# Kernel tuning notes

Hardware: AMD Instinct MI355X
Metric: run time of the kernel (lower is better)

## Reference

```python
import jax, jax.numpy as jnp
import numpy as np

TEMPERATURE = 34.0
PAD = 1  # kernel_size // 2

def setup_inputs() -> dict:
    key = jax.random.key(0)
    ks = jax.random.split(key, 5)
    B, C, H, W = 32, 256, 56, 56
    K, O, I, kh = 4, 256, 256, 3
    hidden = int(C * 0.25) + 1  # 65
    return {
        "x": jax.random.normal(ks[0], (B, C, H, W), jnp.float32),
        "fc1_w": jax.random.normal(ks[1], (hidden, C), jnp.float32) * (2.0 / C) ** 0.5,
        "fc2_w": jax.random.normal(ks[2], (K, hidden), jnp.float32) * (2.0 / hidden) ** 0.5,
        "fc2_b": jnp.zeros((K,), jnp.float32),
        "weight": jax.random.normal(ks[3], (K, O, I, kh, kh), jnp.float32) * (2.0 / (I * kh * kh)) ** 0.5,
        "bias": jnp.zeros((K, O), jnp.float32),
    }

def reference(x, fc1_w, fc2_w, fc2_b, weight, bias):
    # attention2d: global avg pool -> 1x1 conv (fc1) -> relu -> 1x1 conv (fc2) -> softmax(logits/T)
    pooled = x.mean(axis=(2, 3))                      # [B, C]
    h = jax.nn.relu(pooled @ fc1_w.T)                 # [B, hidden]
    logits = h @ fc2_w.T + fc2_b                      # [B, K]
    att = jax.nn.softmax(logits / TEMPERATURE, axis=1)
    # aggregate per-sample conv weights/bias over K kernel banks
    agg_w = jnp.einsum('bk,koihw->boihw', att, weight)  # [B, O, I, kh, kw]
    agg_b = att @ bias                                  # [B, O]
    # per-sample conv (torch emulates via groups=B): vmap over batch
    def conv_one(xi, wi):
        return jax.lax.conv_general_dilated(
            xi[None], wi, window_strides=(1, 1),
            padding=((PAD, PAD), (PAD, PAD)),
            dimension_numbers=('NCHW', 'OIHW', 'NCHW'))[0]
    out = jax.vmap(conv_one)(x, agg_w)                 # [B, O, H, W]
    return out + agg_b[:, :, None, None]
```

## Files before the change

### kernel.cpp

```cpp
#include <hip/hip_runtime.h>


typedef short bf16x8 __attribute__((ext_vector_type(8)));
typedef float f32x16 __attribute__((ext_vector_type(16)));

__device__ __forceinline__ unsigned short f2bf(float f) {
  unsigned int u = __float_as_uint(f);
  return (unsigned short)((u + 0x7FFFu + ((u >> 16) & 1u)) >> 16);
}
__device__ __forceinline__ float bf2f(unsigned short h) {
  return __uint_as_float(((unsigned int)h) << 16);
}

__device__ __forceinline__ int invswz(int S) {
  int b7 = (S >> 7) & 1;
  int b6 = ((S >> 6) & 1) ^ b7;
  int b5 = ((S >> 5) & 1) ^ b6;
  int b4 = ((S >> 4) & 1) ^ b5;
  return (S & ~0x70) | (b4 << 4) | (b5 << 5) | (b6 << 6);
}

typedef const __attribute__((address_space(1))) unsigned int* gas_t;
typedef __attribute__((address_space(3))) unsigned int* las_t;
__device__ __forceinline__ void dma16(const void* g, unsigned lds_addr) {
  __builtin_amdgcn_global_load_lds((gas_t)g, (las_t)(size_t)lds_addr, 16, 0, 0);
}

__global__ void xcast_k(const float* __restrict__ x, unsigned short* __restrict__ xb,
                        float* __restrict__ pooled) {
  __shared__ unsigned short tile[64 * 260];
  int b = blockIdx.y;
  int hw0 = blockIdx.x * 64;
  int t = threadIdx.x;
  int p = t & 15, g = t >> 4;
#pragma unroll
  for (int i = 0; i < 16; ++i) {
    int c = g + 16 * i;
    float4 v = *(const float4*)(x + ((size_t)(b * 256 + c)) * 3136 + hw0 + p * 4);
    tile[(p * 4 + 0) * 260 + c] = f2bf(v.x);
    tile[(p * 4 + 1) * 260 + c] = f2bf(v.y);
    tile[(p * 4 + 2) * 260 + c] = f2bf(v.z);
    tile[(p * 4 + 3) * 260 + c] = f2bf(v.w);
  }
  __syncthreads();
  int lane = t & 63, wq = t >> 6;
  int c4 = lane * 4;
#pragma unroll
  for (int it = 0; it < 16; ++it) {
    int hl = it * 4 + wq;
    ushort4 v = *(const ushort4*)&tile[hl * 260 + c4];
    *(ushort4*)&xb[((size_t)(b * 3136 + hw0 + hl)) * 256 + c4] = v;
  }
  float s = 0.f;
#pragma unroll 16
  for (int hl = 0; hl < 64; ++hl) s += bf2f(tile[hl * 260 + t]);
  atomicAdd(&pooled[b * 256 + t], s * (1.0f / 3136.0f));
}

__global__ void att_k(const float* __restrict__ pooled, const float* __restrict__ fc1,
                      const float* __restrict__ fc2w, const float* __restrict__ fc2b,
                      const float* __restrict__ bias, float* __restrict__ att,
                      float* __restrict__ aggb) {
  int b = blockIdx.x, t = threadIdx.x;
  __shared__ float p[256];
  __shared__ float h[65];
  __shared__ float a4[4];
  for (int i = t; i < 256; i += 64) p[i] = pooled[b * 256 + i];
  __syncthreads();
  for (int j = t; j < 65; j += 64) {
    float s = 0.f;
    for (int c = 0; c < 256; ++c) s += p[c] * fc1[j * 256 + c];
    h[j] = fmaxf(s, 0.f);
  }
  __syncthreads();
  if (t == 0) {
    float lg[4];
    for (int k = 0; k < 4; ++k) {
      float s = fc2b[k];
      for (int j = 0; j < 65; ++j) s += h[j] * fc2w[k * 65 + j];
      lg[k] = s * (1.0f / 34.0f);
    }
    float m = fmaxf(fmaxf(lg[0], lg[1]), fmaxf(lg[2], lg[3]));
    float e0 = expf(lg[0] - m), e1 = expf(lg[1] - m), e2 = expf(lg[2] - m), e3 = expf(lg[3] - m);
    float inv = 1.0f / (e0 + e1 + e2 + e3);
    a4[0] = e0 * inv; a4[1] = e1 * inv; a4[2] = e2 * inv; a4[3] = e3 * inv;
    for (int k = 0; k < 4; ++k) att[b * 4 + k] = a4[k];
  }
  __syncthreads();
  for (int o = t; o < 256; o += 64) {
    float s = 0.f;
    for (int k = 0; k < 4; ++k) s += a4[k] * bias[k * 256 + o];
    aggb[b * 256 + o] = s;
  }
}

__global__ void aggw_k(const float* __restrict__ weight, const float* __restrict__ att,
                       unsigned short* __restrict__ aggw) {
  __shared__ float wl[4 * 2304];
  int o = blockIdx.x, t = threadIdx.x;
  for (int k = 0; k < 4; ++k)
    for (int idx = t; idx < 2304; idx += 256)
      wl[k * 2304 + idx] = weight[((size_t)(k * 256 + o)) * 2304 + idx];
  __syncthreads();
  int ot = o >> 7, ol = o & 127, ic = t >> 4, il = t & 15;
  int b0 = blockIdx.y * 8;
  for (int b = b0; b < b0 + 8; ++b) {
    float a0 = att[b * 4 + 0], a1 = att[b * 4 + 1], a2 = att[b * 4 + 2], a3 = att[b * 4 + 3];
    size_t base = ((size_t)((b * 2 + ot) * 16 + ic)) * (9 * 2048) + ol * 16 + il;
#pragma unroll
    for (int r = 0; r < 9; ++r) {
      float s = a0 * wl[t * 9 + r] + a1 * wl[2304 + t * 9 + r] +
                a2 * wl[4608 + t * 9 + r] + a3 * wl[6912 + t * 9 + r];
      aggw[base + r * 2048] = f2bf(s);
    }
  }
}

#define XBUF 16384

__global__ __launch_bounds__(256, 2) void conv_k(const unsigned short* __restrict__ xb,
                                                 const unsigned short* __restrict__ aggw,
                                                 const float* __restrict__ aggb,
                                                 const float* __restrict__ zerobuf,
                                                 float* __restrict__ out) {
  __shared__ __align__(16) unsigned char lds[2 * XBUF];
  const unsigned ldsbase = (unsigned)(size_t)&lds[0];
  const int t = threadIdx.x;
  const int wid = t >> 6, lane = t & 63, l31 = lane & 31, q = lane >> 5;
  const int wo = wid >> 1, wn = wid & 1;

  int id = blockIdx.x;
  int wgid = (id & 7) * 104 + (id >> 3);
  int bn = wgid % 13;
  int rest = wgid / 13;
  int b = rest >> 1, bo = rest & 1;

  const int o0 = bo * 128;
  const int n0 = bn * 256;
  const int h0 = n0 / 56;

  int bbase[4], nn[4], swz[4][3];
#pragma unroll
  for (int nf = 0; nf < 4; ++nf) {
    int n = n0 + wn * 128 + nf * 32 + l31;
    int h = n / 56, w = n - h * 56;
    nn[nf] = n;
    bbase[nf] = ((h - h0) * 64 + w) * 32 + q * 16;
#pragma unroll
    for (int dw = 0; dw < 3; ++dw) swz[nf][dw] = ((w + dw) & 7) << 4;
  }
  int aoff[2];
#pragma unroll
  for (int mf = 0; mf < 2; ++mf) aoff[mf] = (wo * 64 + mf * 32 + l31) * 32 + q * 16;

  const char* xb_b = (const char*)xb + (size_t)b * 3136 * 512;
  const char* ag_c = (const char*)aggw + (size_t)rest * 589824;

  const char* xg[4];
#pragma unroll
  for (int j = 0; j < 4; ++j) {
    int S = (j * 256 + t) * 16;
    int L = invswz(S);
    int pos = L >> 5, sub = (L >> 4) & 1;
    int row = pos >> 6, col = pos & 63;
    int hg = h0 - 1 + row, wg = col - 1;
    bool valid = (col >= 1 && col <= 56 && hg >= 0 && hg < 56);
    xg[j] = valid ? (xb_b + (size_t)(hg * 56 + wg) * 512 + sub * 16) : (const char*)zerobuf;
  }

  f32x16 acc[2][4];
#pragma unroll
  for (int i = 0; i < 2; ++i)
#pragma unroll
    for (int j = 0; j < 4; ++j)
#pragma unroll
      for (int e = 0; e < 16; ++e) acc[i][j][e] = 0.f;

#pragma unroll
  for (int j = 0; j < 4; ++j) dma16(xg[j], ldsbase + j * 4096 + wid * 1024);
  __syncthreads();

  int cur = 0;
  for (int ic = 0; ic < 16; ++ic) {
    bf16x8 areg[2][9];
    const char* agc = ag_c + (size_t)ic * 36864;
#pragma unroll
    for (int r = 0; r < 9; ++r) {
      areg[0][r] = *(const bf16x8*)(agc + r * 4096 + aoff[0]);
      areg[1][r] = *(const bf16x8*)(agc + r * 4096 + aoff[1]);
    }
    if (ic + 1 < 16) {
#pragma unroll
      for (int j = 0; j < 4; ++j)
        dma16(xg[j] + (ic + 1) * 32, ldsbase + (cur ^ 1) * XBUF + j * 4096 + wid * 1024);
    }
    __builtin_amdgcn_sched_barrier(0);
    const unsigned char* xlds = lds + cur * XBUF;
#pragma unroll
    for (int r = 0; r < 9; ++r) {
      const int dh = r / 3, dw = r % 3;
      bf16x8 b0 = *(const bf16x8*)(xlds + ((bbase[0] + dh * 2048 + dw * 32) ^ swz[0][dw]));
      bf16x8 b1 = *(const bf16x8*)(xlds + ((bbase[1] + dh * 2048 + dw * 32) ^ swz[1][dw]));
      bf16x8 b2 = *(const bf16x8*)(xlds + ((bbase[2] + dh * 2048 + dw * 32) ^ swz[2][dw]));
      bf16x8 b3 = *(const bf16x8*)(xlds + ((bbase[3] + dh * 2048 + dw * 32) ^ swz[3][dw]));
      __builtin_amdgcn_s_setprio(1);
      acc[0][0] = __builtin_amdgcn_mfma_f32_32x32x16_bf16(areg[0][r], b0, acc[0][0], 0, 0, 0);
      acc[0][1] = __builtin_amdgcn_mfma_f32_32x32x16_bf16(areg[0][r], b1, acc[0][1], 0, 0, 0);
      acc[0][2] = __builtin_amdgcn_mfma_f32_32x32x16_bf16(areg[0][r], b2, acc[0][2], 0, 0, 0);
      acc[0][3] = __builtin_amdgcn_mfma_f32_32x32x16_bf16(areg[0][r], b3, acc[0][3], 0, 0, 0);
      acc[1][0] = __builtin_amdgcn_mfma_f32_32x32x16_bf16(areg[1][r], b0, acc[1][0], 0, 0, 0);
      acc[1][1] = __builtin_amdgcn_mfma_f32_32x32x16_bf16(areg[1][r], b1, acc[1][1], 0, 0, 0);
      acc[1][2] = __builtin_amdgcn_mfma_f32_32x32x16_bf16(areg[1][r], b2, acc[1][2], 0, 0, 0);
      acc[1][3] = __builtin_amdgcn_mfma_f32_32x32x16_bf16(areg[1][r], b3, acc[1][3], 0, 0, 0);
      __builtin_amdgcn_s_setprio(0);
    }
    __syncthreads();
    cur ^= 1;
  }

#pragma unroll
  for (int mf = 0; mf < 2; ++mf) {
#pragma unroll
    for (int reg = 0; reg < 16; ++reg) {
      int o = o0 + wo * 64 + mf * 32 + (reg & 3) + 8 * (reg >> 2) + 4 * q;
      float ab = aggb[b * 256 + o];
      float* op = out + ((size_t)(b * 256 + o)) * 3136;
#pragma unroll
      for (int nf = 0; nf < 4; ++nf) {
        if (nn[nf] < 3136) op[nn[nf]] = acc[mf][nf][reg] + ab;
      }
    }
  }
}

extern "C" void kernel_launch(void* const* d_in, const int* in_sizes, int n_in,
                              void* d_out, int out_size, void* d_ws, size_t ws_size,
                              hipStream_t stream) {
  const float* x      = (const float*)d_in[0];
  const float* fc1    = (const float*)d_in[1];
  const float* fc2w   = (const float*)d_in[2];
  const float* fc2b   = (const float*)d_in[3];
  const float* weight = (const float*)d_in[4];
  const float* bias   = (const float*)d_in[5];
  float* out = (float*)d_out;

  char* ws = (char*)d_ws;
  float* pooled         = (float*)(ws);
  float* att            = (float*)(ws + 32768);
  float* aggb           = (float*)(ws + 33280);
  unsigned short* aggw  = (unsigned short*)(ws + 66048);
  unsigned short* xb    = (unsigned short*)(ws + 66048 + 37748736);

  hipMemsetAsync(pooled, 0, 32768, stream);
  xcast_k<<<dim3(49, 32), 256, 0, stream>>>(x, xb, pooled);
  att_k<<<32, 64, 0, stream>>>(pooled, fc1, fc2w, fc2b, bias, att, aggb);
  hipMemsetAsync(pooled, 0, 1024, stream);
  aggw_k<<<dim3(256, 4), 256, 0, stream>>>(weight, att, aggw);
  conv_k<<<832, 256, 0, stream>>>(xb, aggw, aggb, (const float*)pooled, out);
}
```

Measured before the change: 257.1 us.

## Triple-buffer input tiles in LDS and stream weight fragments per tap

Moves the LDS staging of input activations from double to triple buffering, prefetching two channel chunks ahead and waiting only with a partial vmcnt instead of a full syncthreads. The weight fragments are no longer loaded all at once (18 registers of bf16x8) but software-pipelined one tap ahead, which cuts register pressure. The aim is to hide global-memory latency behind MFMA work and keep occupancy, at the cost of 48KB of LDS per block, which may limit blocks per CU. The hand-written vmcnt counting is fragile: the weight global loads also count toward vmcnt, so correctness depends on the compiler's ordering.

```diff
diff --git a/kernel.cpp b/kernel.cpp
--- a/kernel.cpp
+++ b/kernel.cpp
@@ -123,7 +123,7 @@
                                                  const float* __restrict__ aggb,
                                                  const float* __restrict__ zerobuf,
                                                  float* __restrict__ out) {
-  __shared__ __align__(16) unsigned char lds[2 * XBUF];
+  __shared__ __align__(16) unsigned char lds[3 * XBUF];
   const unsigned ldsbase = (unsigned)(size_t)&lds[0];
   const int t = threadIdx.x;
   const int wid = t >> 6, lane = t & 63, l31 = lane & 31, q = lane >> 5;
@@ -178,45 +178,56 @@
 
 #pragma unroll
   for (int j = 0; j < 4; ++j) dma16(xg[j], ldsbase + j * 4096 + wid * 1024);
-  __syncthreads();
+#pragma unroll
+  for (int j = 0; j < 4; ++j) dma16(xg[j] + 32, ldsbase + XBUF + j * 4096 + wid * 1024);
+  asm volatile("s_waitcnt vmcnt(4)" ::: "memory");
+  __builtin_amdgcn_s_barrier();
 
   int cur = 0;
   for (int ic = 0; ic < 16; ++ic) {
-    bf16x8 areg[2][9];
+    if (ic < 15) {
+      int tgt = cur + 2; if (tgt >= 3) tgt -= 3;
+      int icn = ic + 2 < 16 ? ic + 2 : 15;
+#pragma unroll
+      for (int j = 0; j < 4; ++j)
+        dma16(xg[j] + icn * 32, ldsbase + tgt * XBUF + j * 4096 + wid * 1024);
+      __builtin_amdgcn_sched_barrier(0);
+    }
     const char* agc = ag_c + (size_t)ic * 36864;
-#pragma unroll
-    for (int r = 0; r < 9; ++r) {
-      areg[0][r] = *(const bf16x8*)(agc + r * 4096 + aoff[0]);
-      areg[1][r] = *(const bf16x8*)(agc + r * 4096 + aoff[1]);
-    }
-    if (ic + 1 < 16) {
-#pragma unroll
-      for (int j = 0; j < 4; ++j)
-        dma16(xg[j] + (ic + 1) * 32, ldsbase + (cur ^ 1) * XBUF + j * 4096 + wid * 1024);
-    }
-    __builtin_amdgcn_sched_barrier(0);
     const unsigned char* xlds = lds + cur * XBUF;
+    bf16x8 a0c = *(const bf16x8*)(agc + aoff[0]);
+    bf16x8 a1c = *(const bf16x8*)(agc + aoff[1]);
 #pragma unroll
     for (int r = 0; r < 9; ++r) {
       const int dh = r / 3, dw = r % 3;
+      bf16x8 a0n, a1n;
+      if (r < 8) {
+        a0n = *(const bf16x8*)(agc + (r + 1) * 4096 + aoff[0]);
+        a1n = *(const bf16x8*)(agc + (r + 1) * 4096 + aoff[1]);
+      }
       bf16x8 b0 = *(const bf16x8*)(xlds + ((bbase[0] + dh * 2048 + dw * 32) ^ swz[0][dw]));
       bf16x8 b1 = *(const bf16x8*)(xlds + ((bbase[1] + dh * 2048 + dw * 32) ^ swz[1][dw]));
       bf16x8 b2 = *(const bf16x8*)(xlds + ((bbase[2] + dh * 2048 + dw * 32) ^ swz[2][dw]));
       bf16x8 b3 = *(const bf16x8*)(xlds + ((bbase[3] + dh * 2048 + dw * 32) ^ swz[3][dw]));
       __builtin_amdgcn_s_setprio(1);
-      acc[0][0] = __builtin_amdgcn_mfma_f32_32x32x16_bf16(areg[0][r], b0, acc[0][0], 0, 0, 0);
-      acc[0][1] = __builtin_amdgcn_mfma_f32_32x32x16_bf16(areg[0][r], b1, acc[0][1], 0, 0, 0);
-      acc[0][2] = __builtin_amdgcn_mfma_f32_32x32x16_bf16(areg[0][r], b2, acc[0][2], 0, 0, 0);
-      acc[0][3] = __builtin_amdgcn_mfma_f32_32x32x16_bf16(areg[0][r], b3, acc[0][3], 0, 0, 0);
-      acc[1][0] = __builtin_amdgcn_mfma_f32_32x32x16_bf16(areg[1][r], b0, acc[1][0], 0, 0, 0);
-      acc[1][1] = __builtin_amdgcn_mfma_f32_32x32x16_bf16(areg[1][r], b1, acc[1][1], 0, 0, 0);
-      acc[1][2] = __builtin_amdgcn_mfma_f32_32x32x16_bf16(areg[1][r], b2, acc[1][2], 0, 0, 0);
-      acc[1][3] = __builtin_amdgcn_mfma_f32_32x32x16_bf16(areg[1][r], b3, acc[1][3], 0, 0, 0);
+      acc[0][0] = __builtin_amdgcn_mfma_f32_32x32x16_bf16(a0c, b0, acc[0][0], 0, 0, 0);
+      acc[0][1] = __builtin_amdgcn_mfma_f32_32x32x16_bf16(a0c, b1, acc[0][1], 0, 0, 0);
+      acc[0][2] = __builtin_amdgcn_mfma_f32_32x32x16_bf16(a0c, b2, acc[0][2], 0, 0, 0);
+      acc[0][3] = __builtin_amdgcn_mfma_f32_32x32x16_bf16(a0c, b3, acc[0][3], 0, 0, 0);
+      acc[1][0] = __builtin_amdgcn_mfma_f32_32x32x16_bf16(a1c, b0, acc[1][0], 0, 0, 0);
+      acc[1][1] = __builtin_amdgcn_mfma_f32_32x32x16_bf16(a1c, b1, acc[1][1], 0, 0, 0);
+      acc[1][2] = __builtin_amdgcn_mfma_f32_32x32x16_bf16(a1c, b2, acc[1][2], 0, 0, 0);
+      acc[1][3] = __builtin_amdgcn_mfma_f32_32x32x16_bf16(a1c, b3, acc[1][3], 0, 0, 0);
       __builtin_amdgcn_s_setprio(0);
-    }
-    __syncthreads();
-    cur ^= 1;
-  }
+      if (r < 8) { a0c = a0n; a1c = a1n; }
+    }
+    if (ic < 15) {
+      asm volatile("s_waitcnt vmcnt(4)" ::: "memory");
+      __builtin_amdgcn_s_barrier();
+    }
+    cur += 1; if (cur >= 3) cur -= 3;
+  }
+  asm volatile("s_waitcnt vmcnt(0)" ::: "memory");
 
 #pragma unroll
   for (int mf = 0; mf < 2; ++mf) {
```

Measured after the change: 237.5 us. -7.6%, faster.
